# Kernel tuning notes

Measured on AMD Instinct MI355X. Metric: run time of the kernel, lower is better.

The kernel has to match this reference:

```python
import jax, jax.numpy as jnp
import numpy as np

N = 100000   # nodes
E = 640000   # edges
F = 128      # num_features
H = 128      # hidden_channels
EPS = 1e-5   # BatchNorm1d eps
SCALE = 0.05


def setup_inputs() -> dict:
    key = jax.random.key(0)
    ks = jax.random.split(key, 16)
    inp = {
        "x": jax.random.normal(ks[0], (N, F), dtype=jnp.float32),
        "edge_index": jax.random.randint(ks[1], (2, E), 0, N, dtype=jnp.int32),
    }
    dims = [(F, H), (H, H), (H, H)]
    k = 2
    for i, (din, dout) in enumerate(dims):
        inp[f"Wl{i}"] = jax.random.normal(ks[k], (dout, din), dtype=jnp.float32) * SCALE
        inp[f"bl{i}"] = jax.random.normal(ks[k + 1], (dout,), dtype=jnp.float32) * SCALE
        inp[f"Wr{i}"] = jax.random.normal(ks[k + 2], (dout, din), dtype=jnp.float32) * SCALE
        k += 3
    inp["W1"] = jax.random.normal(ks[k], (H, H), dtype=jnp.float32) * SCALE
    inp["b1"] = jax.random.normal(ks[k + 1], (H,), dtype=jnp.float32) * SCALE
    inp["W2"] = jax.random.normal(ks[k + 2], (2, H), dtype=jnp.float32) * SCALE
    inp["b2"] = jax.random.normal(ks[k + 3], (2,), dtype=jnp.float32) * SCALE
    return inp


def _batchnorm(x):
    # BatchNorm1d(track_running_stats=False, affine=False): biased batch stats
    mu = jnp.mean(x, axis=0)
    var = jnp.var(x, axis=0)
    return (x - mu) / jnp.sqrt(var + EPS)


def _sage_conv(x, src, dst, Wl, bl, Wr):
    # PyG SAGEConv (aggr='mean'): out = lin_l(mean_agg(x[src] -> dst)) + lin_r(x)
    msg = x[src]                                             # [E, din]
    ssum = jax.ops.segment_sum(msg, dst, num_segments=N)     # [N, din]
    cnt = jax.ops.segment_sum(jnp.ones((E,), x.dtype), dst, num_segments=N)
    agg = ssum / jnp.maximum(cnt, 1.0)[:, None]              # mean, 0 for isolated
    return agg @ Wl.T + bl + x @ Wr.T


def reference(x, edge_index, Wl0, bl0, Wr0, Wl1, bl1, Wr1, Wl2, bl2, Wr2, W1, b1, W2, b2):
    src, dst = edge_index[0], edge_index[1]
    for Wl, bl, Wr in ((Wl0, bl0, Wr0), (Wl1, bl1, Wr1), (Wl2, bl2, Wr2)):
        x = jax.nn.relu(_batchnorm(_sage_conv(x, src, dst, Wl, bl, Wr)))
    x = jax.nn.relu(_batchnorm(x @ W1.T + b1))
    return x @ W2.T + b2
```

## Files before the change

### kernel.cpp

```cpp
#include <hip/hip_runtime.h>
#include <stdint.h>

typedef __bf16 v8bf __attribute__((ext_vector_type(8)));
typedef float f32x4 __attribute__((ext_vector_type(4)));
typedef float f32x2 __attribute__((ext_vector_type(2)));

__device__ __forceinline__ float b2f(unsigned short u) {
    unsigned int x = ((unsigned int)u) << 16;
    return __builtin_bit_cast(float, x);
}
__device__ __forceinline__ float b2f_lo(unsigned int v) {
    return __builtin_bit_cast(float, v << 16);
}
__device__ __forceinline__ float b2f_hi(unsigned int v) {
    return __builtin_bit_cast(float, v & 0xffff0000u);
}
__device__ __forceinline__ unsigned short f2b(float f) {
    unsigned int x = __builtin_bit_cast(unsigned int, f);
    unsigned int r = (x + 0x7fffu + ((x >> 16) & 1u)) >> 16;
    return (unsigned short)r;
}

__device__ __forceinline__ void load_lds16(const void* g, void* l) {
    __builtin_amdgcn_global_load_lds(
        (__attribute__((address_space(1))) void*)(const void*)g,
        (__attribute__((address_space(3))) void*)l, 16, 0, 0);
}

#define VMW(n) asm volatile("s_waitcnt vmcnt(" #n ")" ::: "memory")

struct WSrc { const float* p[7]; const float* s[6]; };

__global__ void k_prologue(WSrc w, unsigned short* __restrict__ wbuf,
                           const int* __restrict__ src, const int* __restrict__ dst,
                           int* __restrict__ pos, int* __restrict__ csr, int E,
                           const float* __restrict__ x, unsigned short* __restrict__ xcat,
                           unsigned short* __restrict__ ya, unsigned short* __restrict__ yb,
                           int n, int nFill, int nCvtw, int nCopyx) {
    int bid = blockIdx.x;
    int t = threadIdx.x;
    if (bid < nFill) {
        int i = bid * 256 + t;
        if (i < E) {
            int d = dst[i];
            int p = atomicAdd(&pos[d], 1);
            if (p < 64) csr[((size_t)d << 6) + p] = src[i];
        }
    } else if (bid < nFill + nCvtw) {
        int idx = (bid - nFill) * 256 + t;
        if (idx < 115458) {
            float v;
            if (idx < 114688) {
                v = w.p[idx >> 14][idx & 16383];
            } else {
                int rem = idx - 114688;
                int tt, j;
                if (rem < 512)      { tt = rem >> 7; j = rem & 127; }
                else if (rem < 768) { tt = 4; j = rem - 512; }
                else                { tt = 5; j = rem - 768; }
                v = w.s[tt][j];
            }
            wbuf[idx] = f2b(v);
        } else if (idx < 115458 + 96) {
            int k = idx - 115458;
            if (k < 32) {
                ushort4 z; z.x = z.y = z.z = z.w = 0;
                *(ushort4*)&xcat[(size_t)n * 256 + 128 + k * 4] = z;
            } else if (k < 64) {
                ushort4 m; m.x = m.y = m.z = m.w = 0xFF7Fu;
                *(ushort4*)&ya[(size_t)n * 128 + (k - 32) * 4] = m;
            } else {
                ushort4 m; m.x = m.y = m.z = m.w = 0xFF7Fu;
                *(ushort4*)&yb[(size_t)n * 128 + (k - 64) * 4] = m;
            }
        }
    } else {
        int T = nCopyx * 256;
        int tid = (bid - nFill - nCvtw) * 256 + t;
        int total = n * 32;
        for (int i0 = tid; i0 < total; i0 += 4 * T) {
#pragma unroll
            for (int u = 0; u < 4; u++) {
                int i = i0 + u * T;
                if (i < total) {
                    int row = i >> 5, c4 = (i & 31) * 4;
                    float4 v = *(const float4*)&x[(size_t)row * 128 + c4];
                    ushort4 o;
                    o.x = f2b(v.x); o.y = f2b(v.y); o.z = f2b(v.z); o.w = f2b(v.w);
                    *(ushort4*)&xcat[(size_t)row * 256 + 128 + c4] = o;
                }
            }
        }
    }
}

template<bool BN>
__global__ __launch_bounds__(256, 3) void k_fused(const unsigned short* __restrict__ S, int slda, int soff,
                                                  const float* __restrict__ statp,
                                                  const int* __restrict__ cnt, const int* __restrict__ csr,
                                                  const unsigned short* __restrict__ W0,
                                                  const unsigned short* __restrict__ W1,
                                                  const unsigned short* __restrict__ bias,
                                                  unsigned short* __restrict__ Y,
                                                  float* __restrict__ statp_out,
                                                  int n, float invN) {
    __shared__ __align__(16) unsigned short As[8][1024];
    __shared__ float smu[128], sinv[128], sq[128];
    int t = threadIdx.x;
    int wv = t >> 6, lane = t & 63;
    int quad = lane >> 4, l16 = lane & 15;
    int grp = t >> 4;
    int l = t & 15;
    int gbase = (t & 63) & ~15;

    if constexpr (BN) {
        if (t < 128) {
            float s = 0.f;
#pragma unroll
            for (int sl = 0; sl < 32; sl++) s += statp[sl * 256 + t];
            smu[t] = s * invN;
        } else {
            int u = t - 128;
            float q = 0.f;
#pragma unroll
            for (int sl = 0; sl < 32; sl++) q += statp[sl * 256 + 128 + u];
            sq[u] = q;
        }
        __syncthreads();
        if (t < 128) {
            float mu = smu[t];
            sinv[t] = rsqrtf(sq[t] * invN - mu * mu + 1e-5f);
        }
        __syncthreads();
    }

    v8bf wreg[8][2];
#pragma unroll
    for (int c = 0; c < 8; c++) {
        const unsigned short* Wp = (c < 4) ? W0 : W1;
#pragma unroll
        for (int j = 0; j < 2; j++)
            wreg[c][j] = *(const v8bf*)(Wp + (size_t)(wv * 32 + j * 16 + l16) * 128 + (c & 3) * 32 + quad * 8);
    }
    float bn[2][4];
#pragma unroll
    for (int j = 0; j < 2; j++) {
        int c0 = wv * 32 + j * 16 + quad * 4;
        uint2 bu = *(const uint2*)&bias[c0];
        bn[j][0] = b2f_lo(bu.x); bn[j][1] = b2f_hi(bu.x);
        bn[j][2] = b2f_lo(bu.y); bn[j][3] = b2f_hi(bu.y);
    }

    f32x2 mu2[4];
    float iv8[8];
    if constexpr (BN) {
#pragma unroll
        for (int k = 0; k < 4; k++) {
            mu2[k].x = smu[l * 8 + 2 * k];
            mu2[k].y = smu[l * 8 + 2 * k + 1];
        }
#pragma unroll
        for (int k = 0; k < 8; k++) iv8[k] = sinv[l * 8 + k];
    }

    f32x4 cs_[2] = {}, cq_[2] = {};
    int ntiles = (n + 31) >> 5;

    for (int mt = blockIdx.x; mt < ntiles; mt += (int)gridDim.x) {
        int m0 = mt * 32;
#pragma unroll
        for (int p = 0; p < 2; p++) {
            int r = p * 16 + grp;
            int d = m0 + r;
            int dd = (d < n) ? d : (n - 1);
            uint4 vo = *(const uint4*)(S + (size_t)dd * slda + soff + l * 8);
            uint4 ow;
            if constexpr (BN) {
                unsigned int uu[4] = {vo.x, vo.y, vo.z, vo.w};
                unsigned int* op = (unsigned int*)&ow;
#pragma unroll
                for (int k = 0; k < 4; k++) {
                    float a = fmaxf((b2f_lo(uu[k]) - mu2[k].x) * iv8[2 * k], 0.f);
                    float b = fmaxf((b2f_hi(uu[k]) - mu2[k].y) * iv8[2 * k + 1], 0.f);
                    op[k] = ((unsigned int)f2b(b) << 16) | f2b(a);
                }
            } else {
                ow = vo;
            }
            *(uint4*)&As[4 + (l >> 2)][r * 32 + (l & 3) * 8] = ow;
            int deg = (d < n) ? cnt[dd] : 0;
            size_t s = (size_t)dd << 6;
            f32x2 z2 = {0.f, 0.f};
            f32x2 ax[4] = {};
            for (int base = 0; base < deg; base += 16) {
                int myidx = (base + l < deg) ? csr[s + base + l] : n;
                int lim = min(16, deg - base);
                for (int b = 0; b < lim; b += 8) {
                    int idx[8];
                    uint4 v[8];
#pragma unroll
                    for (int u = 0; u < 8; u++) idx[u] = __shfl(myidx, gbase + b + u, 64);
#pragma unroll
                    for (int u = 0; u < 8; u++)
                        v[u] = *(const uint4*)(S + (size_t)(unsigned)idx[u] * slda + soff + (unsigned)(l << 3));
#pragma unroll
                    for (int u = 0; u < 8; u++) {
                        unsigned int uu[4] = {v[u].x, v[u].y, v[u].z, v[u].w};
#pragma unroll
                        for (int k = 0; k < 4; k++) {
                            f32x2 tv;
                            tv.x = b2f_lo(uu[k]);
                            tv.y = b2f_hi(uu[k]);
                            if constexpr (BN) {
                                tv = tv - mu2[k];
                                tv = __builtin_elementwise_max(tv, z2);
                            }
                            ax[k] += tv;
                        }
                    }
                }
            }
            float ic = 1.0f / (float)max(deg, 1);
            uint4 ag;
            unsigned int* ap = (unsigned int*)&ag;
            if constexpr (BN) {
#pragma unroll
                for (int k = 0; k < 4; k++)
                    ap[k] = ((unsigned int)f2b(ax[k].y * (iv8[2 * k + 1] * ic)) << 16)
                          | f2b(ax[k].x * (iv8[2 * k] * ic));
            } else {
#pragma unroll
                for (int k = 0; k < 4; k++)
                    ap[k] = ((unsigned int)f2b(ax[k].y * ic) << 16) | f2b(ax[k].x * ic);
            }
            *(uint4*)&As[l >> 2][r * 32 + (l & 3) * 8] = ag;
        }
        __syncthreads();

        f32x4 acc[2][2] = {};
#pragma unroll
        for (int c = 0; c < 8; c++) {
            v8bf af0 = *(const v8bf*)&As[c][(l16) * 32 + quad * 8];
            v8bf af1 = *(const v8bf*)&As[c][(16 + l16) * 32 + quad * 8];
            acc[0][0] = __builtin_amdgcn_mfma_f32_16x16x32_bf16(wreg[c][0], af0, acc[0][0], 0, 0, 0);
            acc[0][1] = __builtin_amdgcn_mfma_f32_16x16x32_bf16(wreg[c][1], af0, acc[0][1], 0, 0, 0);
            acc[1][0] = __builtin_amdgcn_mfma_f32_16x16x32_bf16(wreg[c][0], af1, acc[1][0], 0, 0, 0);
            acc[1][1] = __builtin_amdgcn_mfma_f32_16x16x32_bf16(wreg[c][1], af1, acc[1][1], 0, 0, 0);
        }
#pragma unroll
        for (int i = 0; i < 2; i++)
#pragma unroll
            for (int j = 0; j < 2; j++)
#pragma unroll
                for (int u = 0; u < 4; u++)
                    acc[i][j][u] += bn[j][u];
#pragma unroll
        for (int i = 0; i < 2; i++) {
            int row = m0 + i * 16 + l16;
            int srow = (row < n) ? row : (n + 1);
#pragma unroll
            for (int j = 0; j < 2; j++) {
                int c0 = wv * 32 + j * 16 + quad * 4;
                uint2 o;
                o.x = ((unsigned int)f2b(acc[i][j][1]) << 16) | f2b(acc[i][j][0]);
                o.y = ((unsigned int)f2b(acc[i][j][3]) << 16) | f2b(acc[i][j][2]);
                *(uint2*)&Y[(size_t)srow * 128 + c0] = o;
            }
        }
#pragma unroll
        for (int i = 0; i < 2; i++) {
            int row = m0 + i * 16 + l16;
            if (row < n) {
#pragma unroll
                for (int j = 0; j < 2; j++)
#pragma unroll
                    for (int u = 0; u < 4; u++) {
                        float v = acc[i][j][u];
                        cs_[j][u] += v;
                        cq_[j][u] += v * v;
                    }
            }
        }
        __syncthreads();
    }

    float* sp = statp_out + (blockIdx.x & 31) * 256;
#pragma unroll
    for (int j = 0; j < 2; j++) {
        for (int m = 1; m < 16; m <<= 1) {
#pragma unroll
            for (int u = 0; u < 4; u++) {
                cs_[j][u] += __shfl_xor(cs_[j][u], m, 64);
                cq_[j][u] += __shfl_xor(cq_[j][u], m, 64);
            }
        }
        if (l16 == 0) {
            int c0 = wv * 32 + j * 16 + quad * 4;
#pragma unroll
            for (int u = 0; u < 4; u++) {
                atomicAdd(&sp[c0 + u], cs_[j][u]);
                atomicAdd(&sp[128 + c0 + u], cq_[j][u]);
            }
        }
    }
}

__global__ __launch_bounds__(256) void k_wgemm_bn(const unsigned short* __restrict__ A,
                                                  const float* __restrict__ statp,
                                                  const unsigned short* __restrict__ W0,
                                                  const unsigned short* __restrict__ bias,
                                                  unsigned short* __restrict__ Y,
                                                  float* __restrict__ statp_out,
                                                  int nrows, float invN) {
    __shared__ __align__(16) unsigned short Ws[4][4096];
    __shared__ __align__(16) unsigned short As[4][1024];
    __shared__ float smu[128], sinv[128], sq[128];
    int t = threadIdx.x;
    int wv = t >> 6, lane = t & 63;
    int quad = lane >> 4, l16 = lane & 15;

    for (int c = 0; c < 4; c++) {
        int wkc = c * 32;
#pragma unroll
        for (int q = 0; q < 2; q++) {
            int r = q * 64 + (t >> 2);
            load_lds16(W0 + (size_t)r * 128 + wkc + (t & 3) * 8,
                       &Ws[c][(size_t)r * 32 + (t & 3) * 8]);
        }
    }

    if (t < 128) {
        float s = 0.f;
#pragma unroll
        for (int sl = 0; sl < 32; sl++) s += statp[sl * 256 + t];
        smu[t] = s * invN;
    } else {
        int u = t - 128;
        float q = 0.f;
#pragma unroll
        for (int sl = 0; sl < 32; sl++) q += statp[sl * 256 + 128 + u];
        sq[u] = q;
    }
    __syncthreads();
    if (t < 128) {
        float mu = smu[t];
        sinv[t] = rsqrtf(sq[t] * invN - mu * mu + 1e-5f);
    }
    __syncthreads();

    int c16 = (t & 15) * 8;
    int sch = (t & 15) >> 2;
    int sac = (t & 3) * 8;
    int sr = t >> 4;
    float mu8[8], iv8[8];
#pragma unroll
    for (int k = 0; k < 8; k++) { mu8[k] = smu[c16 + k]; iv8[k] = sinv[c16 + k]; }

    float bn[2][4];
#pragma unroll
    for (int j = 0; j < 2; j++) {
        int c0 = wv * 32 + j * 16 + quad * 4;
        uint2 bu = *(const uint2*)&bias[c0];
        bn[j][0] = b2f_lo(bu.x); bn[j][1] = b2f_hi(bu.x);
        bn[j][2] = b2f_lo(bu.y); bn[j][3] = b2f_hi(bu.y);
    }

    f32x4 cs_[2] = {}, cq_[2] = {};

    int ntiles = (nrows + 31) >> 5;
    int mt = blockIdx.x;
    uint4 ra0, ra1;
    {
        int g0 = min(mt * 32 + sr, nrows - 1);
        int g1 = min(mt * 32 + 16 + sr, nrows - 1);
        ra0 = *(const uint4*)(A + (size_t)g0 * 128 + c16);
        ra1 = *(const uint4*)(A + (size_t)g1 * 128 + c16);
    }
    auto xf = [&](uint4 v) -> uint4 {
        unsigned int uu[4] = {v.x, v.y, v.z, v.w};
        uint4 o; unsigned int* op = (unsigned int*)&o;
#pragma unroll
        for (int k = 0; k < 4; k++) {
            float a = fmaxf((b2f_lo(uu[k]) - mu8[2 * k]) * iv8[2 * k], 0.f);
            float b = fmaxf((b2f_hi(uu[k]) - mu8[2 * k + 1]) * iv8[2 * k + 1], 0.f);
            op[k] = ((unsigned int)f2b(b) << 16) | f2b(a);
        }
        return o;
    };

    for (; mt < ntiles; mt += (int)gridDim.x) {
        int m0 = mt * 32;
        int nxt = mt + (int)gridDim.x;

        VMW(0);
        __builtin_amdgcn_sched_barrier(0);
        __builtin_amdgcn_s_barrier();
        __builtin_amdgcn_sched_barrier(0);
        *(uint4*)&As[sch][(size_t)sr * 32 + sac] = xf(ra0);
        *(uint4*)&As[sch][(size_t)(16 + sr) * 32 + sac] = xf(ra1);
        __syncthreads();

        if (nxt < ntiles) {
            int g0 = min(nxt * 32 + sr, nrows - 1);
            int g1 = min(nxt * 32 + 16 + sr, nrows - 1);
            ra0 = *(const uint4*)(A + (size_t)g0 * 128 + c16);
            ra1 = *(const uint4*)(A + (size_t)g1 * 128 + c16);
        }

        f32x4 acc[2][2] = {};
#pragma unroll
        for (int c = 0; c < 4; c++) {
            v8bf af[2], bfv[2];
#pragma unroll
            for (int i = 0; i < 2; i++)
                af[i] = *(const v8bf*)&As[c][(i * 16 + l16) * 32 + quad * 8];
#pragma unroll
            for (int j = 0; j < 2; j++)
                bfv[j] = *(const v8bf*)&Ws[c][(wv * 32 + j * 16 + l16) * 32 + quad * 8];
#pragma unroll
            for (int i = 0; i < 2; i++)
#pragma unroll
                for (int j = 0; j < 2; j++)
                    acc[i][j] = __builtin_amdgcn_mfma_f32_16x16x32_bf16(bfv[j], af[i], acc[i][j], 0, 0, 0);
        }

#pragma unroll
        for (int i = 0; i < 2; i++)
#pragma unroll
            for (int j = 0; j < 2; j++)
#pragma unroll
                for (int u = 0; u < 4; u++)
                    acc[i][j][u] += bn[j][u];
#pragma unroll
        for (int i = 0; i < 2; i++) {
            int row = m0 + i * 16 + l16;
            int srow = (row < nrows) ? row : (nrows + 1);
#pragma unroll
            for (int j = 0; j < 2; j++) {
                int c0 = wv * 32 + j * 16 + quad * 4;
                uint2 o;
                o.x = ((unsigned int)f2b(acc[i][j][1]) << 16) | f2b(acc[i][j][0]);
                o.y = ((unsigned int)f2b(acc[i][j][3]) << 16) | f2b(acc[i][j][2]);
                *(uint2*)&Y[(size_t)srow * 128 + c0] = o;
            }
        }
#pragma unroll
        for (int i = 0; i < 2; i++) {
            int row = m0 + i * 16 + l16;
            if (row < nrows) {
#pragma unroll
                for (int j = 0; j < 2; j++)
#pragma unroll
                    for (int u = 0; u < 4; u++) {
                        float v = acc[i][j][u];
                        cs_[j][u] += v;
                        cq_[j][u] += v * v;
                    }
            }
        }
    }

    float* sp = statp_out + (blockIdx.x & 31) * 256;
#pragma unroll
    for (int j = 0; j < 2; j++) {
        for (int m = 1; m < 16; m <<= 1) {
#pragma unroll
            for (int u = 0; u < 4; u++) {
                cs_[j][u] += __shfl_xor(cs_[j][u], m, 64);
                cq_[j][u] += __shfl_xor(cq_[j][u], m, 64);
            }
        }
        if (l16 == 0) {
            int c0 = wv * 32 + j * 16 + quad * 4;
#pragma unroll
            for (int u = 0; u < 4; u++) {
                atomicAdd(&sp[c0 + u], cs_[j][u]);
                atomicAdd(&sp[128 + c0 + u], cq_[j][u]);
            }
        }
    }
}

__global__ __launch_bounds__(256) void k_bnfinal(const unsigned short* __restrict__ Y,
                                                 const float* __restrict__ statp,
                                                 const unsigned short* __restrict__ W2,
                                                 const unsigned short* __restrict__ b2v,
                                                 float* __restrict__ out, int n, float invN) {
    __shared__ float smu[128], sinv[128], sq[128];
    int t = threadIdx.x;
    if (t < 128) {
        float s = 0.f;
#pragma unroll
        for (int sl = 0; sl < 32; sl++) s += statp[sl * 256 + t];
        smu[t] = s * invN;
    } else {
        int u = t - 128;
        float q = 0.f;
#pragma unroll
        for (int sl = 0; sl < 32; sl++) q += statp[sl * 256 + 128 + u];
        sq[u] = q;
    }
    __syncthreads();
    if (t < 128) {
        float mu = smu[t];
        sinv[t] = rsqrtf(sq[t] * invN - mu * mu + 1e-5f);
    }
    __syncthreads();
    int l = t & 15;
    int r = blockIdx.x * 16 + (t >> 4);
    if (r >= n) return;
    int f8 = l * 8;
    uint4 v = *(const uint4*)&Y[(size_t)r * 128 + f8];
    uint4 w0v = *(const uint4*)&W2[f8];
    uint4 w1v = *(const uint4*)&W2[128 + f8];
    unsigned int uu[4] = {v.x, v.y, v.z, v.w};
    unsigned int u0[4] = {w0v.x, w0v.y, w0v.z, w0v.w};
    unsigned int u1[4] = {w1v.x, w1v.y, w1v.z, w1v.w};
    float d0 = 0.f, d1 = 0.f;
#pragma unroll
    for (int k = 0; k < 4; k++) {
        int f = f8 + 2 * k;
        float a = fmaxf((b2f_lo(uu[k]) - smu[f]) * sinv[f], 0.f);
        float b = fmaxf((b2f_hi(uu[k]) - smu[f + 1]) * sinv[f + 1], 0.f);
        d0 += a * b2f_lo(u0[k]) + b * b2f_hi(u0[k]);
        d1 += a * b2f_lo(u1[k]) + b * b2f_hi(u1[k]);
    }
    for (int o = 1; o < 16; o <<= 1) {
        d0 += __shfl_xor(d0, o, 64);
        d1 += __shfl_xor(d1, o, 64);
    }
    if (l == 0) {
        float2 o2;
        o2.x = d0 + b2f(b2v[0]);
        o2.y = d1 + b2f(b2v[1]);
        *(float2*)&out[(size_t)r * 2] = o2;
    }
}

extern "C" void kernel_launch(void* const* d_in, const int* in_sizes, int n_in,
                              void* d_out, int out_size, void* d_ws, size_t ws_size,
                              hipStream_t stream) {
    const int N = in_sizes[0] / 128;
    const int E = in_sizes[1] / 2;

    const float* x = (const float*)d_in[0];
    const int* ei = (const int*)d_in[1];
    const int* srcp = ei;
    const int* dstp = ei + E;
    float* out = (float*)d_out;

    char* w = (char*)d_ws;
    auto align256 = [](size_t v) { return (v + 255) & ~(size_t)255; };
    size_t o_xcat = 0;
    size_t o_ya   = align256(o_xcat + (size_t)(N + 1) * 256 * 2);
    size_t o_yb   = align256(o_ya + (size_t)(N + 2) * 128 * 2);
    size_t o_csr  = align256(o_yb + (size_t)(N + 2) * 128 * 2);
    size_t o_wbuf = align256(o_csr + (size_t)N * 64 * 4);
    size_t o_pos  = align256(o_wbuf + 115712 * 2);
    size_t o_stat = o_pos + (size_t)N * 4;

    unsigned short* xcat = (unsigned short*)(w + o_xcat);
    unsigned short* ya   = (unsigned short*)(w + o_ya);
    unsigned short* yb   = (unsigned short*)(w + o_yb);
    int* csr = (int*)(w + o_csr);
    unsigned short* wbuf = (unsigned short*)(w + o_wbuf);
    int* pos = (int*)(w + o_pos);
    float* stat = (float*)(w + o_stat);

    const unsigned short* Wl[3] = {wbuf + 0,      wbuf + 32768, wbuf + 65536};
    const unsigned short* Wr[3] = {wbuf + 16384,  wbuf + 49152, wbuf + 81920};
    const unsigned short* W1b   = wbuf + 98304;
    const unsigned short* bl[3] = {wbuf + 114688, wbuf + 114816, wbuf + 114944};
    const unsigned short* b1b   = wbuf + 115072;
    const unsigned short* W2b   = wbuf + 115200;
    const unsigned short* b2b   = wbuf + 115456;

    WSrc wsrc;
    wsrc.p[0] = (const float*)d_in[2];
    wsrc.p[1] = (const float*)d_in[4];
    wsrc.p[2] = (const float*)d_in[5];
    wsrc.p[3] = (const float*)d_in[7];
    wsrc.p[4] = (const float*)d_in[8];
    wsrc.p[5] = (const float*)d_in[10];
    wsrc.p[6] = (const float*)d_in[11];
    wsrc.s[0] = (const float*)d_in[3];
    wsrc.s[1] = (const float*)d_in[6];
    wsrc.s[2] = (const float*)d_in[9];
    wsrc.s[3] = (const float*)d_in[12];
    wsrc.s[4] = (const float*)d_in[13];
    wsrc.s[5] = (const float*)d_in[14];

    const int nFill = (E + 255) / 256;
    const int nCvtw = (115458 + 96 + 255) / 256;
    const int nCopyx = 1024;

    hipMemsetAsync(w + o_pos, 0, (size_t)N * 4 + 4 * 8192 * 4, stream);

    k_prologue<<<nFill + nCvtw + nCopyx, 256, 0, stream>>>(wsrc, wbuf, srcp, dstp, pos, csr, E,
                                                           x, xcat, ya, yb, N, nFill, nCvtw, nCopyx);

    const int fgrid = 768;
    const int row16_grid = (N + 15) / 16;
    const float invN = 1.0f / (float)N;

    k_fused<false><<<fgrid, 256, 0, stream>>>(xcat, 256, 128, nullptr, pos, csr,
                                              Wl[0], Wr[0], bl[0], ya, stat + 0 * 8192, N, invN);
    k_fused<true><<<fgrid, 256, 0, stream>>>(ya, 128, 0, stat + 0 * 8192, pos, csr,
                                             Wl[1], Wr[1], bl[1], yb, stat + 1 * 8192, N, invN);
    k_fused<true><<<fgrid, 256, 0, stream>>>(yb, 128, 0, stat + 1 * 8192, pos, csr,
                                             Wl[2], Wr[2], bl[2], ya, stat + 2 * 8192, N, invN);
    k_wgemm_bn<<<512, 256, 0, stream>>>(ya, stat + 2 * 8192, W1b, b1b, ya, stat + 3 * 8192, N, invN);
    k_bnfinal<<<row16_grid, 256, 0, stream>>>(ya, stat + 3 * 8192, W2b, b2b, out, N, invN);
}
```

Baseline: 328.5 us.

## Spread neighbor gather across whole wavefront with shuffle reduction, raise occupancy

The mean-aggregation gather is remapped. Previously each 16-lane group walked one destination row's neighbor list 8 at a time. Now a full 64-lane wave processes one row at a time: four 16-lane slots fetch different neighbors in parallel, and the partial sums are combined with cross-slot shuffle reductions before one slot writes the tile. This cuts padded loads on low-degree rows and spreads each row's latency across more lanes, at the cost of extra shuffles and serializing 8 rows per wave. Launch bounds are raised to 4 blocks per SM and the grid to 1024 to increase occupancy, which may add register pressure.

```diff
diff --git a/kernel.cpp b/kernel.cpp
--- a/kernel.cpp
+++ b/kernel.cpp
@@ -95,7 +95,7 @@
 }
 
 template<bool BN>
-__global__ __launch_bounds__(256, 3) void k_fused(const unsigned short* __restrict__ S, int slda, int soff,
+__global__ __launch_bounds__(256, 4) void k_fused(const unsigned short* __restrict__ S, int slda, int soff,
                                                   const float* __restrict__ statp,
                                                   const int* __restrict__ cnt, const int* __restrict__ csr,
                                                   const unsigned short* __restrict__ W0,
@@ -111,7 +111,6 @@
     int quad = lane >> 4, l16 = lane & 15;
     int grp = t >> 4;
     int l = t & 15;
-    int gbase = (t & 63) & ~15;
 
     if constexpr (BN) {
         if (t < 128) {
@@ -165,6 +164,8 @@
 
     f32x4 cs_[2] = {}, cq_[2] = {};
     int ntiles = (n + 31) >> 5;
+    int slot = lane >> 4;
+    f32x2 z2 = {0.f, 0.f};
 
     for (int mt = blockIdx.x; mt < ntiles; mt += (int)gridDim.x) {
         int m0 = mt * 32;
@@ -188,52 +189,60 @@
                 ow = vo;
             }
             *(uint4*)&As[4 + (l >> 2)][r * 32 + (l & 3) * 8] = ow;
+        }
+        for (int r8 = 0; r8 < 8; r8++) {
+            int r = wv * 8 + r8;
+            int d = m0 + r;
+            int dd = (d < n) ? d : (n - 1);
             int deg = (d < n) ? cnt[dd] : 0;
             size_t s = (size_t)dd << 6;
-            f32x2 z2 = {0.f, 0.f};
+            int myidx = (lane < deg) ? csr[s + lane] : n;
             f32x2 ax[4] = {};
-            for (int base = 0; base < deg; base += 16) {
-                int myidx = (base + l < deg) ? csr[s + base + l] : n;
-                int lim = min(16, deg - base);
-                for (int b = 0; b < lim; b += 8) {
-                    int idx[8];
-                    uint4 v[8];
-#pragma unroll
-                    for (int u = 0; u < 8; u++) idx[u] = __shfl(myidx, gbase + b + u, 64);
-#pragma unroll
-                    for (int u = 0; u < 8; u++)
-                        v[u] = *(const uint4*)(S + (size_t)(unsigned)idx[u] * slda + soff + (unsigned)(l << 3));
-#pragma unroll
-                    for (int u = 0; u < 8; u++) {
-                        unsigned int uu[4] = {v[u].x, v[u].y, v[u].z, v[u].w};
-#pragma unroll
-                        for (int k = 0; k < 4; k++) {
-                            f32x2 tv;
-                            tv.x = b2f_lo(uu[k]);
-                            tv.y = b2f_hi(uu[k]);
-                            if constexpr (BN) {
-                                tv = tv - mu2[k];
-                                tv = __builtin_elementwise_max(tv, z2);
-                            }
-                            ax[k] += tv;
-                        }
+            for (int it = 0; it < deg; it += 8) {
+                int i0 = __shfl(myidx, it + slot, 64);
+                int i1 = __shfl(myidx, it + 4 + slot, 64);
+                uint4 v0 = *(const uint4*)(S + (size_t)(unsigned)i0 * slda + soff + (unsigned)(l << 3));
+                uint4 v1 = *(const uint4*)(S + (size_t)(unsigned)i1 * slda + soff + (unsigned)(l << 3));
+                unsigned int uu0[4] = {v0.x, v0.y, v0.z, v0.w};
+                unsigned int uu1[4] = {v1.x, v1.y, v1.z, v1.w};
+#pragma unroll
+                for (int k = 0; k < 4; k++) {
+                    f32x2 ta, tb;
+                    ta.x = b2f_lo(uu0[k]); ta.y = b2f_hi(uu0[k]);
+                    tb.x = b2f_lo(uu1[k]); tb.y = b2f_hi(uu1[k]);
+                    if constexpr (BN) {
+                        ta = ta - mu2[k];
+                        tb = tb - mu2[k];
+                        ta = __builtin_elementwise_max(ta, z2);
+                        tb = __builtin_elementwise_max(tb, z2);
                     }
+                    ax[k] += ta;
+                    ax[k] += tb;
                 }
             }
-            float ic = 1.0f / (float)max(deg, 1);
-            uint4 ag;
-            unsigned int* ap = (unsigned int*)&ag;
-            if constexpr (BN) {
-#pragma unroll
-                for (int k = 0; k < 4; k++)
-                    ap[k] = ((unsigned int)f2b(ax[k].y * (iv8[2 * k + 1] * ic)) << 16)
-                          | f2b(ax[k].x * (iv8[2 * k] * ic));
-            } else {
-#pragma unroll
-                for (int k = 0; k < 4; k++)
-                    ap[k] = ((unsigned int)f2b(ax[k].y * ic) << 16) | f2b(ax[k].x * ic);
-            }
-            *(uint4*)&As[l >> 2][r * 32 + (l & 3) * 8] = ag;
+#pragma unroll
+            for (int k = 0; k < 4; k++) {
+                ax[k].x += __shfl_xor(ax[k].x, 16, 64);
+                ax[k].y += __shfl_xor(ax[k].y, 16, 64);
+                ax[k].x += __shfl_xor(ax[k].x, 32, 64);
+                ax[k].y += __shfl_xor(ax[k].y, 32, 64);
+            }
+            if (slot == 0) {
+                float ic = 1.0f / (float)max(deg, 1);
+                uint4 ag;
+                unsigned int* ap = (unsigned int*)&ag;
+                if constexpr (BN) {
+#pragma unroll
+                    for (int k = 0; k < 4; k++)
+                        ap[k] = ((unsigned int)f2b(ax[k].y * (iv8[2 * k + 1] * ic)) << 16)
+                              | f2b(ax[k].x * (iv8[2 * k] * ic));
+                } else {
+#pragma unroll
+                    for (int k = 0; k < 4; k++)
+                        ap[k] = ((unsigned int)f2b(ax[k].y * ic) << 16) | f2b(ax[k].x * ic);
+                }
+                *(uint4*)&As[l >> 2][r * 32 + (l & 3) * 8] = ag;
+            }
         }
         __syncthreads();
 
@@ -599,7 +608,7 @@
     k_prologue<<<nFill + nCvtw + nCopyx, 256, 0, stream>>>(wsrc, wbuf, srcp, dstp, pos, csr, E,
                                                            x, xcat, ya, yb, N, nFill, nCvtw, nCopyx);
 
-    const int fgrid = 768;
+    const int fgrid = 1024;
     const int row16_grid = (N + 15) / 16;
     const float invN = 1.0f / (float)N;
 
```

Result: slower. 450.8 us (+37.2%).
